# Optimization experiments

Hardware: AMD Instinct MI355X
Metric: run time of the kernel (lower is better)

## Reference

```python
import jax, jax.numpy as jnp
import numpy as np

N_NODES = 50000
N_EDGES = 800000
IN_DIM = 128
HID = 2 * IN_DIM          # GCNConv out channels = input_dims * 2
FC1 = 1024
FC2 = 512
N_ACT = 16
N_AGENTS = 8192
EPS = 1e-5


def setup_inputs() -> dict:
    key = jax.random.key(0)
    ks = jax.random.split(key, 12)
    def gl(k, shape):  # glorot-ish init for weights
        fan = shape[0]
        return jax.random.normal(k, shape, jnp.float32) / jnp.sqrt(jnp.float32(fan))
    return {
        "x": jax.random.normal(ks[0], (N_NODES, IN_DIM), jnp.float32),
        "edge_index": jax.random.randint(ks[1], (2, N_EDGES), 0, N_NODES, jnp.int32),
        "agent_idx": jax.random.randint(ks[2], (N_AGENTS,), 0, N_NODES, jnp.int32),
        "W_gcn": gl(ks[3], (IN_DIM, HID)),
        "b_gcn": jnp.zeros((HID,), jnp.float32),
        "W1": gl(ks[4], (HID, FC1)),
        "b1": jnp.zeros((FC1,), jnp.float32),
        "g1": jnp.ones((FC1,), jnp.float32),
        "be1": jnp.zeros((FC1,), jnp.float32),
        "W2": gl(ks[5], (FC1, FC2)),
        "b2": jnp.zeros((FC2,), jnp.float32),
        "g2": jnp.ones((FC2,), jnp.float32),
        "be2": jnp.zeros((FC2,), jnp.float32),
        "Wmu": gl(ks[6], (FC2, N_ACT)) * 0.003,
        "bmu": jnp.zeros((N_ACT,), jnp.float32),
    }


def _layernorm(h, g, b):
    mu = jnp.mean(h, axis=-1, keepdims=True)
    var = jnp.mean(jnp.square(h - mu), axis=-1, keepdims=True)
    return (h - mu) * jax.lax.rsqrt(var + EPS) * g + b


def _gcn_conv(x, edge_index, W, b):
    # PyG GCNConv: add self-loops, symmetric normalization, linear, scatter-add.
    n = x.shape[0]
    loop = jnp.arange(n, dtype=edge_index.dtype)
    src = jnp.concatenate([edge_index[0], loop])   # [E+N]
    dst = jnp.concatenate([edge_index[1], loop])   # [E+N]
    deg = jax.ops.segment_sum(jnp.ones_like(dst, jnp.float32), dst, num_segments=n)
    dis = jnp.where(deg > 0, jax.lax.rsqrt(jnp.maximum(deg, 1.0)), 0.0)
    norm = dis[src] * dis[dst]                     # [E+N]
    xw = x @ W                                     # [N, HID]
    msg = xw[src] * norm[:, None]                  # gather + scale
    return jax.ops.segment_sum(msg, dst, num_segments=n) + b


def reference(x, edge_index, agent_idx, W_gcn, b_gcn, W1, b1, g1, be1,
              W2, b2, g2, be2, Wmu, bmu):
    h = _gcn_conv(x, edge_index, W_gcn, b_gcn)     # [N, HID]
    h = h[agent_idx]                               # masked selection -> [A, HID]
    h = jax.nn.relu(h)
    h = jax.nn.relu(_layernorm(h @ W1 + b1, g1, be1))
    h = jax.nn.relu(_layernorm(h @ W2 + b2, g2, be2))
    return jax.nn.sigmoid(h @ Wmu + bmu)           # [A, N_ACT]
```

## Files before the change

### kernel.cpp

```cpp
#include <hip/hip_runtime.h>
#include <hip/hip_bf16.h>
#include <math.h>

#define N_NODES  50000
#define N_EDGES  800000
#define IN_DIM   128
#define HID      256
#define FC1      1024
#define FC2      512
#define N_ACT    16
#define N_AGENTS 8192

#define BK       64
#define BM       128
#define BN       128

#define EB_STRIDE    64

#define SCAT_CHUNK   2048
#define SCAT_BLOCKS  ((N_EDGES + SCAT_CHUNK - 1) / SCAT_CHUNK)
#define N_BUCKETS    196
#define BUCKET_CAP   4608
#define WTR_BLOCKS   208
#define CLAIM_BLOCKS (N_AGENTS / 256)

typedef short bf16x8 __attribute__((ext_vector_type(8)));
typedef float floatx4 __attribute__((ext_vector_type(4)));

__device__ __forceinline__ unsigned short f2b(float f) {
    union { float f; unsigned int i; } v;
    v.f = f;
    unsigned int lsb = (v.i >> 16) & 1u;
    v.i += 0x7fffu + lsb;
    return (unsigned short)(v.i >> 16);
}

__device__ __forceinline__ float b2f(unsigned short u) {
    union { unsigned int i; float f; } v;
    v.i = ((unsigned int)u) << 16;
    return v.f;
}

__device__ __forceinline__ void gl_lds(const unsigned short* g, unsigned short* l) {
    __builtin_amdgcn_global_load_lds(
        (const __attribute__((address_space(1))) void*)g,
        (__attribute__((address_space(3))) void*)l, 16, 0, 0);
}

__device__ __forceinline__ void wtr_block(int b, int tid,
    const float* __restrict__ Wgcn, const float* __restrict__ W1,
    const float* __restrict__ W2, const float* __restrict__ Wmu,
    unsigned short* __restrict__ wgcn_t, unsigned short* __restrict__ w1_t,
    unsigned short* __restrict__ w2_t, unsigned short* __restrict__ wmu_t,
    unsigned short (*Ts)[72]) {
    const float* src; unsigned short* dstw; int K, N, tk, tn;
    if (b < 8)        { src = Wgcn; dstw = wgcn_t; K = IN_DIM; N = HID;  tk = b >> 2;        tn = b & 3; }
    else if (b < 72)  { int bb = b - 8;  src = W1; dstw = w1_t; K = HID;  N = FC1;  tk = bb >> 4; tn = bb & 15; }
    else if (b < 200) { int bb = b - 72; src = W2; dstw = w2_t; K = FC1;  N = FC2;  tk = bb >> 3; tn = bb & 7; }
    else              { int bb = b - 200; src = Wmu; dstw = wmu_t; K = FC2; N = N_ACT; tk = bb;   tn = 0; }
    int k0 = tk * 64, n0 = tn * 64;
    int r = tid >> 2;
    int cc = (tid & 3) * 16;
    if (n0 + cc < N) {
        const float* p = src + (size_t)(k0 + r) * N + n0 + cc;
        #pragma unroll
        for (int i = 0; i < 16; i += 4) {
            float4 v = *(const float4*)(p + i);
            Ts[r][cc + i + 0] = f2b(v.x);
            Ts[r][cc + i + 1] = f2b(v.y);
            Ts[r][cc + i + 2] = f2b(v.z);
            Ts[r][cc + i + 3] = f2b(v.w);
        }
    }
    __syncthreads();
    int n = tid >> 2;
    if (n0 + n < N) {
        bf16x8 o0, o1;
        #pragma unroll
        for (int i = 0; i < 8; ++i) o0[i] = (short)Ts[cc + i][n];
        #pragma unroll
        for (int i = 0; i < 8; ++i) o1[i] = (short)Ts[cc + 8 + i][n];
        unsigned short* q = dstw + (size_t)(n0 + n) * K + k0 + cc;
        *(bf16x8*)q = o0;
        *(bf16x8*)(q + 8) = o1;
    }
}

__global__ __launch_bounds__(256) void scat_k(const int* __restrict__ src,
                                              const int* __restrict__ dst,
                                              const int* __restrict__ agent_idx,
                                              int* __restrict__ nid,
                                              int* __restrict__ bcnt,
                                              unsigned long long* __restrict__ pairbuf,
                                              const float* __restrict__ Wgcn,
                                              const float* __restrict__ W1,
                                              const float* __restrict__ W2,
                                              const float* __restrict__ Wmu,
                                              unsigned short* __restrict__ wgcn_t,
                                              unsigned short* __restrict__ w1_t,
                                              unsigned short* __restrict__ w2_t,
                                              unsigned short* __restrict__ wmu_t) {
    __shared__ unsigned short Ts[64][72];
    __shared__ int hist[N_BUCKETS], base_[N_BUCKETS], cur[N_BUCKETS];
    int tid = threadIdx.x;
    int blk = blockIdx.x;
    if (blk >= SCAT_BLOCKS) {
        int bb = blk - SCAT_BLOCKS;
        if (bb < WTR_BLOCKS) {
            wtr_block(bb, tid, Wgcn, W1, W2, Wmu, wgcn_t, w1_t, w2_t, wmu_t, Ts);
        } else {
            int i = (bb - WTR_BLOCKS) * 256 + tid;
            atomicCAS(&nid[agent_idx[i]], 0, i + 1);
        }
        return;
    }
    if (tid < N_BUCKETS) { hist[tid] = 0; cur[tid] = 0; }
    __syncthreads();
    int e0 = blk * SCAT_CHUNK;
    int dv[8];
    #pragma unroll
    for (int i = 0; i < 8; ++i) {
        int e = e0 + i * 256 + tid;
        dv[i] = (e < N_EDGES) ? dst[e] : -1;
        if (dv[i] >= 0) atomicAdd(&hist[dv[i] >> 8], 1);
    }
    __syncthreads();
    if (tid < N_BUCKETS && hist[tid] > 0)
        base_[tid] = atomicAdd(&bcnt[tid], hist[tid]);
    __syncthreads();
    #pragma unroll
    for (int i = 0; i < 8; ++i) {
        int e = e0 + i * 256 + tid;
        if (e < N_EDGES) {
            int d = dv[i];
            int bk = d >> 8;
            int p = base_[bk] + atomicAdd(&cur[bk], 1);
            if (p < BUCKET_CAP)
                pairbuf[(size_t)bk * BUCKET_CAP + p] =
                    ((unsigned long long)(unsigned)src[e] << 32) | (unsigned)d;
        }
    }
}

__global__ __launch_bounds__(256) void bucket_k(const int* __restrict__ bcnt,
                                                const unsigned long long* __restrict__ pairbuf,
                                                const int* __restrict__ nid,
                                                int* __restrict__ deg,
                                                int* __restrict__ ebuf) {
    __shared__ int nidl[256], lhist[256], lfill[256];
    int b = blockIdx.x, tid = threadIdx.x;
    int node = b * 256 + tid;
    nidl[tid] = (node < N_NODES) ? nid[node] : 0;
    lhist[tid] = 0;
    lfill[tid] = 0;
    __syncthreads();
    int n = bcnt[b];
    if (n > BUCKET_CAP) n = BUCKET_CAP;
    const unsigned long long* pb = pairbuf + (size_t)b * BUCKET_CAP;
    for (int i = tid; i < n; i += 256) {
        unsigned long long pr = pb[i];
        int d = (int)(unsigned)pr;
        int s = (int)(pr >> 32);
        int l = d & 255;
        atomicAdd(&lhist[l], 1);
        int cc = nidl[l];
        if (cc != 0) {
            int p = atomicAdd(&lfill[l], 1);
            if (p < EB_STRIDE) ebuf[((cc - 1) << 6) + p] = s;
        }
    }
    __syncthreads();
    if (node < N_NODES) deg[node] = lhist[tid];
}

__global__ __launch_bounds__(256) void accumx_k(const int* __restrict__ agent_idx,
                                                const int* __restrict__ nid,
                                                const int* __restrict__ deg,
                                                const int* __restrict__ ebuf,
                                                const float* __restrict__ x,
                                                unsigned short* __restrict__ agg) {
    int c = blockIdx.x * 4 + (threadIdx.x >> 6);
    int lane = threadIdx.x & 63;
    int n = agent_idx[c];
    float ax = 0.0f, ay = 0.0f;
    if (nid[n] == c + 1) {
        int dn_i = deg[n];
        int cnt = dn_i < EB_STRIDE ? dn_i : EB_STRIDE;
        float dn = rsqrtf((float)(dn_i + 1));
        const int* eb = ebuf + (c << 6);
        int ej = (lane < cnt) ? eb[lane] : n;
        float wl = rsqrtf((float)(deg[ej] + 1)) * dn;
        const float* xl = x + lane * 2;
        int i = 0;
        for (; i + 4 <= cnt; i += 4) {
            int s0 = __shfl(ej, i),     s1 = __shfl(ej, i + 1);
            int s2 = __shfl(ej, i + 2), s3 = __shfl(ej, i + 3);
            float w0 = __shfl(wl, i),     w1 = __shfl(wl, i + 1);
            float w2 = __shfl(wl, i + 2), w3 = __shfl(wl, i + 3);
            float2 u0 = *(const float2*)(xl + (size_t)s0 * IN_DIM);
            float2 u1 = *(const float2*)(xl + (size_t)s1 * IN_DIM);
            float2 u2 = *(const float2*)(xl + (size_t)s2 * IN_DIM);
            float2 u3 = *(const float2*)(xl + (size_t)s3 * IN_DIM);
            ax += w0 * u0.x; ay += w0 * u0.y;
            ax += w1 * u1.x; ay += w1 * u1.y;
            ax += w2 * u2.x; ay += w2 * u2.y;
            ax += w3 * u3.x; ay += w3 * u3.y;
        }
        for (; i < cnt; ++i) {
            int s = __shfl(ej, i);
            float w = __shfl(wl, i);
            float2 u = *(const float2*)(xl + (size_t)s * IN_DIM);
            ax += w * u.x;
            ay += w * u.y;
        }
        float2 u = *(const float2*)(xl + (size_t)n * IN_DIM);
        float w2s = dn * dn;
        ax += w2s * u.x;
        ay += w2s * u.y;
    }
    unsigned int pk = (unsigned int)f2b(ax) | ((unsigned int)f2b(ay) << 16);
    *(unsigned int*)(agg + (size_t)c * IN_DIM + lane * 2) = pk;
}


__global__ __launch_bounds__(256) void gemm_gcn_k(const unsigned short* __restrict__ A,
                                                  const unsigned short* __restrict__ Bt,
                                                  const float* __restrict__ bias,
                                                  unsigned short* __restrict__ outb) {
    __shared__ unsigned short As[64][64];
    __shared__ unsigned short Bs[128][64];
    int bid = blockIdx.x;
    int tn = (bid >> 3) & 1;
    int tm = (bid & 7) + 8 * (bid >> 4);
    int tid = threadIdx.x;
    int lane = tid & 63, wave = tid >> 6;
    int r16 = lane & 15, quad = lane >> 4;
    int lr = (tid >> 3) & 7;
    int swz = ((tid & 7) ^ lr) * 8;
    const int K = IN_DIM, N = HID;

    floatx4 acc[4][2];
    #pragma unroll
    for (int i = 0; i < 4; ++i)
        #pragma unroll
        for (int j = 0; j < 2; ++j)
            acc[i][j] = (floatx4){0.0f, 0.0f, 0.0f, 0.0f};

    for (int k0 = 0; k0 < K; k0 += BK) {
        if (k0) __syncthreads();
        #pragma unroll
        for (int q = 0; q < 2; ++q)
            gl_lds(A + (size_t)(tm * 64 + (wave * 2 + q) * 8 + lr) * K + k0 + swz,
                   &As[(wave * 2 + q) * 8][0]);
        #pragma unroll
        for (int q = 0; q < 4; ++q)
            gl_lds(Bt + (size_t)(tn * 128 + (wave * 4 + q) * 8 + lr) * K + k0 + swz,
                   &Bs[(wave * 4 + q) * 8][0]);
        __syncthreads();
        #pragma unroll
        for (int h = 0; h < 2; ++h) {
            int col = (h * 32 + quad * 8) ^ ((r16 & 7) << 3);
            bf16x8 af[4], bfr[2];
            #pragma unroll
            for (int i = 0; i < 4; ++i)
                af[i] = *(const bf16x8*)&As[i * 16 + r16][col];
            #pragma unroll
            for (int j = 0; j < 2; ++j)
                bfr[j] = *(const bf16x8*)&Bs[wave * 32 + j * 16 + r16][col];
            #pragma unroll
            for (int i = 0; i < 4; ++i)
                #pragma unroll
                for (int j = 0; j < 2; ++j)
                    acc[i][j] = __builtin_amdgcn_mfma_f32_16x16x32_bf16(af[i], bfr[j], acc[i][j], 0, 0, 0);
        }
    }

    #pragma unroll
    for (int j = 0; j < 2; ++j) {
        int ocol = tn * 128 + wave * 32 + j * 16 + r16;
        float bv = bias[ocol];
        #pragma unroll
        for (int i = 0; i < 4; ++i) {
            int orow = tm * 64 + i * 16 + quad * 4;
            #pragma unroll
            for (int r = 0; r < 4; ++r) {
                float v = acc[i][j][r] + bv;
                if (v < 0.0f) v = 0.0f;
                outb[(size_t)(orow + r) * N + ocol] = f2b(v);
            }
        }
    }
}

__global__ __launch_bounds__(256) void gemm_fc1_k(const unsigned short* __restrict__ h_node,
                                                  const int* __restrict__ agent,
                                                  const int* __restrict__ nid,
                                                  const unsigned short* __restrict__ Bt,
                                                  const float* __restrict__ bias,
                                                  unsigned short* __restrict__ outb) {
    __shared__ unsigned short As[BM][64];
    __shared__ unsigned short Bs[BN][64];
    int bid = blockIdx.x;
    int tn = (bid >> 3) & 7;
    int tm = (bid & 7) + 8 * (bid >> 6);
    int tid = threadIdx.x;
    int lane = tid & 63, wave = tid >> 6;
    int wm = wave >> 1, wn = wave & 1;
    int r16 = lane & 15, quad = lane >> 4;
    int lr = (tid >> 3) & 7;
    int swz = ((tid & 7) ^ lr) * 8;
    const int K = HID, N = FC1;

    int cA[4];
    #pragma unroll
    for (int q = 0; q < 4; ++q)
        cA[q] = nid[agent[tm * BM + (wave * 4 + q) * 8 + lr]] - 1;

    floatx4 acc[4][4];
    #pragma unroll
    for (int i = 0; i < 4; ++i)
        #pragma unroll
        for (int j = 0; j < 4; ++j)
            acc[i][j] = (floatx4){0.0f, 0.0f, 0.0f, 0.0f};

    for (int k0 = 0; k0 < K; k0 += BK) {
        if (k0) __syncthreads();
        #pragma unroll
        for (int q = 0; q < 4; ++q) {
            gl_lds(h_node + (size_t)cA[q] * K + k0 + swz,
                   &As[(wave * 4 + q) * 8][0]);
            gl_lds(Bt + (size_t)(tn * BN + (wave * 4 + q) * 8 + lr) * K + k0 + swz,
                   &Bs[(wave * 4 + q) * 8][0]);
        }
        __syncthreads();
        #pragma unroll
        for (int h = 0; h < 2; ++h) {
            int col = (h * 32 + quad * 8) ^ ((r16 & 7) << 3);
            bf16x8 af[4], bfr[4];
            #pragma unroll
            for (int i = 0; i < 4; ++i)
                af[i] = *(const bf16x8*)&As[wm * 64 + i * 16 + r16][col];
            #pragma unroll
            for (int j = 0; j < 4; ++j)
                bfr[j] = *(const bf16x8*)&Bs[wn * 64 + j * 16 + r16][col];
            #pragma unroll
            for (int i = 0; i < 4; ++i)
                #pragma unroll
                for (int j = 0; j < 4; ++j)
                    acc[i][j] = __builtin_amdgcn_mfma_f32_16x16x32_bf16(af[i], bfr[j], acc[i][j], 0, 0, 0);
        }
    }

    float bvj[4];
    #pragma unroll
    for (int j = 0; j < 4; ++j) bvj[j] = bias[tn * BN + wn * 64 + j * 16 + r16];

    #pragma unroll
    for (int i = 0; i < 4; ++i) {
        #pragma unroll
        for (int r = 0; r < 4; ++r) {
            int orow = tm * BM + wm * 64 + i * 16 + quad * 4 + r;
            #pragma unroll
            for (int j = 0; j < 4; ++j) {
                int ocol = tn * BN + wn * 64 + j * 16 + r16;
                outb[(size_t)orow * N + ocol] = f2b(acc[i][j][r] + bvj[j]);
            }
        }
    }
}

__global__ __launch_bounds__(256) void ln1_k(const unsigned short* __restrict__ zb,
                                             const float* __restrict__ g1,
                                             const float* __restrict__ be1,
                                             unsigned short* __restrict__ zbn) {
    int row = blockIdx.x * 4 + (threadIdx.x >> 6);
    int lane = threadIdx.x & 63;
    const unsigned short* p = zb + (size_t)row * FC1 + lane * 16;
    bf16x8 a0 = *(const bf16x8*)p;
    bf16x8 a1 = *(const bf16x8*)(p + 8);
    float v[16];
    #pragma unroll
    for (int i = 0; i < 8; ++i) {
        v[i]     = b2f((unsigned short)a0[i]);
        v[8 + i] = b2f((unsigned short)a1[i]);
    }
    float s = 0.0f, s2 = 0.0f;
    #pragma unroll
    for (int i = 0; i < 16; ++i) { s += v[i]; s2 += v[i] * v[i]; }
    #pragma unroll
    for (int m = 1; m < 64; m <<= 1) {
        s  += __shfl_xor(s, m);
        s2 += __shfl_xor(s2, m);
    }
    float mean = s * (1.0f / FC1);
    float var = s2 * (1.0f / FC1) - mean * mean;
    float inv = rsqrtf(var + 1e-5f);
    const float4* g4 = (const float4*)(g1 + lane * 16);
    const float4* b4 = (const float4*)(be1 + lane * 16);
    float gg[16], bb[16];
    #pragma unroll
    for (int q = 0; q < 4; ++q) {
        float4 gv = g4[q], bv = b4[q];
        gg[q * 4 + 0] = gv.x; gg[q * 4 + 1] = gv.y; gg[q * 4 + 2] = gv.z; gg[q * 4 + 3] = gv.w;
        bb[q * 4 + 0] = bv.x; bb[q * 4 + 1] = bv.y; bb[q * 4 + 2] = bv.z; bb[q * 4 + 3] = bv.w;
    }
    bf16x8 o0, o1;
    #pragma unroll
    for (int i = 0; i < 8; ++i) {
        float w = (v[i] - mean) * inv * gg[i] + bb[i];
        if (w < 0.0f) w = 0.0f;
        o0[i] = (short)f2b(w);
    }
    #pragma unroll
    for (int i = 0; i < 8; ++i) {
        float w = (v[8 + i] - mean) * inv * gg[8 + i] + bb[8 + i];
        if (w < 0.0f) w = 0.0f;
        o1[i] = (short)f2b(w);
    }
    unsigned short* q = zbn + (size_t)row * FC1 + lane * 16;
    *(bf16x8*)q = o0;
    *(bf16x8*)(q + 8) = o1;
}

__global__ __launch_bounds__(256) void gemm_fc2_k(const unsigned short* __restrict__ A,
                                                  const unsigned short* __restrict__ Bt,
                                                  const float* __restrict__ bias,
                                                  unsigned short* __restrict__ outb) {
    __shared__ unsigned short As[BM][64];
    __shared__ unsigned short Bs[BN][64];
    int bid = blockIdx.x;
    int tn = (bid >> 3) & 3;
    int tm = (bid & 7) + 8 * (bid >> 5);
    int tid = threadIdx.x;
    int lane = tid & 63, wave = tid >> 6;
    int wm = wave >> 1, wn = wave & 1;
    int r16 = lane & 15, quad = lane >> 4;
    int lr = (tid >> 3) & 7;
    int swz = ((tid & 7) ^ lr) * 8;
    const int K = FC1, N = FC2;

    floatx4 acc[4][4];
    #pragma unroll
    for (int i = 0; i < 4; ++i)
        #pragma unroll
        for (int j = 0; j < 4; ++j)
            acc[i][j] = (floatx4){0.0f, 0.0f, 0.0f, 0.0f};

    for (int k0 = 0; k0 < K; k0 += BK) {
        if (k0) __syncthreads();
        #pragma unroll
        for (int q = 0; q < 4; ++q) {
            gl_lds(A + (size_t)(tm * BM + (wave * 4 + q) * 8 + lr) * K + k0 + swz,
                   &As[(wave * 4 + q) * 8][0]);
            gl_lds(Bt + (size_t)(tn * BN + (wave * 4 + q) * 8 + lr) * K + k0 + swz,
                   &Bs[(wave * 4 + q) * 8][0]);
        }
        __syncthreads();
        #pragma unroll
        for (int h = 0; h < 2; ++h) {
            int col = (h * 32 + quad * 8) ^ ((r16 & 7) << 3);
            bf16x8 af[4], bfr[4];
            #pragma unroll
            for (int i = 0; i < 4; ++i)
                af[i] = *(const bf16x8*)&As[wm * 64 + i * 16 + r16][col];
            #pragma unroll
            for (int j = 0; j < 4; ++j)
                bfr[j] = *(const bf16x8*)&Bs[wn * 64 + j * 16 + r16][col];
            #pragma unroll
            for (int i = 0; i < 4; ++i)
                #pragma unroll
                for (int j = 0; j < 4; ++j)
                    acc[i][j] = __builtin_amdgcn_mfma_f32_16x16x32_bf16(af[i], bfr[j], acc[i][j], 0, 0, 0);
        }
    }

    float bvj[4];
    #pragma unroll
    for (int j = 0; j < 4; ++j) bvj[j] = bias[tn * BN + wn * 64 + j * 16 + r16];

    #pragma unroll
    for (int i = 0; i < 4; ++i) {
        #pragma unroll
        for (int r = 0; r < 4; ++r) {
            int orow = tm * BM + wm * 64 + i * 16 + quad * 4 + r;
            #pragma unroll
            for (int j = 0; j < 4; ++j) {
                int ocol = tn * BN + wn * 64 + j * 16 + r16;
                outb[(size_t)orow * N + ocol] = f2b(acc[i][j][r] + bvj[j]);
            }
        }
    }
}

__global__ __launch_bounds__(256) void ln2head_k(const unsigned short* __restrict__ z,
                                                 const float* __restrict__ g2,
                                                 const float* __restrict__ be2,
                                                 const unsigned short* __restrict__ wmu_t,
                                                 const float* __restrict__ bmu,
                                                 float* __restrict__ out) {
    __shared__ unsigned short Hs[16][520];
    __shared__ float hred[4][64][4];
    int tid = threadIdx.x;
    int tm = blockIdx.x;
    {
        int row = tid >> 4;
        int sub = tid & 15;
        const unsigned short* src = z + (size_t)(tm * 16 + row) * FC2 + sub * 32;
        bf16x8 a0 = *(const bf16x8*)(src);
        bf16x8 a1 = *(const bf16x8*)(src + 8);
        bf16x8 a2 = *(const bf16x8*)(src + 16);
        bf16x8 a3 = *(const bf16x8*)(src + 24);
        float v[32];
        #pragma unroll
        for (int i = 0; i < 8; ++i) {
            v[i]      = b2f((unsigned short)a0[i]);
            v[8 + i]  = b2f((unsigned short)a1[i]);
            v[16 + i] = b2f((unsigned short)a2[i]);
            v[24 + i] = b2f((unsigned short)a3[i]);
        }
        float s = 0.0f, s2 = 0.0f;
        #pragma unroll
        for (int i = 0; i < 32; ++i) { s += v[i]; s2 += v[i] * v[i]; }
        #pragma unroll
        for (int m = 1; m < 16; m <<= 1) {
            s  += __shfl_xor(s, m);
            s2 += __shfl_xor(s2, m);
        }
        float mean = s * (1.0f / FC2);
        float var = s2 * (1.0f / FC2) - mean * mean;
        float inv = rsqrtf(var + 1e-5f);
        #pragma unroll
        for (int i = 0; i < 32; ++i) {
            int c = sub * 32 + i;
            float w = (v[i] - mean) * inv * g2[c] + be2[c];
            if (w < 0.0f) w = 0.0f;
            Hs[row][c] = f2b(w);
        }
    }
    __syncthreads();
    int lane = tid & 63, wave = tid >> 6;
    int r16 = lane & 15, quad = lane >> 4;
    floatx4 acc = {0.0f, 0.0f, 0.0f, 0.0f};
    #pragma unroll
    for (int st = 0; st < 4; ++st) {
        bf16x8 a = *(const bf16x8*)&Hs[r16][wave * 128 + st * 32 + quad * 8];
        bf16x8 b = *(const bf16x8*)(wmu_t + (size_t)r16 * FC2 + wave * 128 + st * 32 + quad * 8);
        acc = __builtin_amdgcn_mfma_f32_16x16x32_bf16(a, b, acc, 0, 0, 0);
    }
    #pragma unroll
    for (int r = 0; r < 4; ++r) hred[wave][lane][r] = acc[r];
    __syncthreads();
    if (wave == 0) {
        #pragma unroll
        for (int r = 0; r < 4; ++r) {
            float v = hred[0][lane][r] + hred[1][lane][r] + hred[2][lane][r] + hred[3][lane][r];
            v += bmu[r16];
            v = 1.0f / (1.0f + expf(-v));
            out[(size_t)(tm * 16 + quad * 4 + r) * N_ACT + r16] = v;
        }
    }
}

extern "C" void kernel_launch(void* const* d_in, const int* in_sizes, int n_in,
                              void* d_out, int out_size, void* d_ws, size_t ws_size,
                              hipStream_t stream) {
    const float* x    = (const float*)d_in[0];
    const int*   ei   = (const int*)d_in[1];
    const int*   agent= (const int*)d_in[2];
    const float* Wgcn = (const float*)d_in[3];
    const float* bgcn = (const float*)d_in[4];
    const float* W1   = (const float*)d_in[5];
    const float* b1   = (const float*)d_in[6];
    const float* g1   = (const float*)d_in[7];
    const float* be1  = (const float*)d_in[8];
    const float* W2   = (const float*)d_in[9];
    const float* b2   = (const float*)d_in[10];
    const float* g2   = (const float*)d_in[11];
    const float* be2  = (const float*)d_in[12];
    const float* Wmu  = (const float*)d_in[13];
    const float* bmu  = (const float*)d_in[14];
    float* out = (float*)d_out;

    const int* srcp = ei;
    const int* dstp = ei + N_EDGES;

    char* ws = (char*)d_ws;
    size_t off = 0;
    char* zero_base = ws;
    int* nid  = (int*)(ws + off);      off += ((size_t)N_NODES * 4 + 255) & ~(size_t)255;
    int* bcnt = (int*)(ws + off);      off += ((size_t)N_BUCKETS * 4 + 255) & ~(size_t)255;
    size_t zero_bytes = off;
    int* deg  = (int*)(ws + off);      off += ((size_t)N_NODES * 4 + 255) & ~(size_t)255;
    unsigned long long* pairbuf = (unsigned long long*)(ws + off);
    off += ((size_t)N_BUCKETS * BUCKET_CAP * 8 + 255) & ~(size_t)255;
    int* ebuf = (int*)(ws + off);      off += ((size_t)N_AGENTS * EB_STRIDE * 4 + 255) & ~(size_t)255;
    unsigned short* wgcn_t = (unsigned short*)(ws + off); off += ((size_t)IN_DIM * HID * 2 + 255) & ~(size_t)255;
    unsigned short* w1_t   = (unsigned short*)(ws + off); off += ((size_t)HID * FC1 * 2 + 255) & ~(size_t)255;
    unsigned short* w2_t   = (unsigned short*)(ws + off); off += ((size_t)FC1 * FC2 * 2 + 255) & ~(size_t)255;
    unsigned short* wmu_t  = (unsigned short*)(ws + off); off += ((size_t)FC2 * N_ACT * 2 + 255) & ~(size_t)255;
    unsigned short* agg    = (unsigned short*)(ws + off); off += ((size_t)N_AGENTS * IN_DIM * 2 + 255) & ~(size_t)255;
    unsigned short* h_node = (unsigned short*)(ws + off); off += ((size_t)N_AGENTS * HID * 2 + 255) & ~(size_t)255;
    unsigned short* zb  = (unsigned short*)(ws + off);    off += ((size_t)N_AGENTS * FC1 * 2 + 255) & ~(size_t)255;
    unsigned short* zbn = (unsigned short*)(ws + off);    off += ((size_t)N_AGENTS * FC1 * 2 + 255) & ~(size_t)255;
    unsigned short* zb2 = (unsigned short*)(ws + off);    off += ((size_t)N_AGENTS * FC2 * 2 + 255) & ~(size_t)255;

    hipMemsetAsync(zero_base, 0, zero_bytes, stream);

    scat_k<<<SCAT_BLOCKS + WTR_BLOCKS + CLAIM_BLOCKS, 256, 0, stream>>>(
        srcp, dstp, agent, nid, bcnt, pairbuf,
        Wgcn, W1, W2, Wmu, wgcn_t, w1_t, w2_t, wmu_t);

    bucket_k<<<N_BUCKETS, 256, 0, stream>>>(bcnt, pairbuf, nid, deg, ebuf);

    accumx_k<<<N_AGENTS / 4, 256, 0, stream>>>(agent, nid, deg, ebuf, x, agg);

    gemm_gcn_k<<<(HID / 128) * (N_AGENTS / 64), 256, 0, stream>>>(agg, wgcn_t, bgcn, h_node);

    gemm_fc1_k<<<(FC1 / BN) * (N_AGENTS / BM), 256, 0, stream>>>(h_node, agent, nid, w1_t, b1, zb);

    ln1_k<<<N_AGENTS / 4, 256, 0, stream>>>(zb, g1, be1, zbn);

    gemm_fc2_k<<<(FC2 / 128) * (N_AGENTS / 128), 256, 0, stream>>>(zbn, w2_t, b2, zb2);

    ln2head_k<<<N_AGENTS / 16, 256, 0, stream>>>(zb2, g2, be2, wmu_t, bmu, out);
}
```

Before: 180.5 us.

## Fuse LayerNorm1 into FC2 GEMM via FC1 epilogue partial stats; pack edge pairs

The FC1 GEMM epilogue now computes per-row partial sums and sums of squares and writes them to a small stats buffer. The FC2 GEMM reads those stats, applies LayerNorm, affine and ReLU on the fly while staging A into LDS, and prefetches the next A tile in registers. This removes the separate ln1 kernel and the extra write and read of the normalized activation. Separately, the edge bucket buffer now packs source id and local destination into 32 bits instead of 64, halving that traffic. The cost is that the A operand in FC2 no longer uses the direct global-to-LDS path and does per-element normalization math that is repeated for every N tile.

```diff
diff --git a/kernel.cpp b/kernel.cpp
--- a/kernel.cpp
+++ b/kernel.cpp
@@ -91,7 +91,7 @@
                                               const int* __restrict__ agent_idx,
                                               int* __restrict__ nid,
                                               int* __restrict__ bcnt,
-                                              unsigned long long* __restrict__ pairbuf,
+                                              unsigned int* __restrict__ pairbuf,
                                               const float* __restrict__ Wgcn,
                                               const float* __restrict__ W1,
                                               const float* __restrict__ W2,
@@ -137,13 +137,13 @@
             int p = base_[bk] + atomicAdd(&cur[bk], 1);
             if (p < BUCKET_CAP)
                 pairbuf[(size_t)bk * BUCKET_CAP + p] =
-                    ((unsigned long long)(unsigned)src[e] << 32) | (unsigned)d;
+                    ((unsigned int)src[e] << 8) | (unsigned int)(d & 255);
         }
     }
 }
 
 __global__ __launch_bounds__(256) void bucket_k(const int* __restrict__ bcnt,
-                                                const unsigned long long* __restrict__ pairbuf,
+                                                const unsigned int* __restrict__ pairbuf,
                                                 const int* __restrict__ nid,
                                                 int* __restrict__ deg,
                                                 int* __restrict__ ebuf) {
@@ -156,12 +156,11 @@
     __syncthreads();
     int n = bcnt[b];
     if (n > BUCKET_CAP) n = BUCKET_CAP;
-    const unsigned long long* pb = pairbuf + (size_t)b * BUCKET_CAP;
+    const unsigned int* pb = pairbuf + (size_t)b * BUCKET_CAP;
     for (int i = tid; i < n; i += 256) {
-        unsigned long long pr = pb[i];
-        int d = (int)(unsigned)pr;
-        int s = (int)(pr >> 32);
-        int l = d & 255;
+        unsigned int pr = pb[i];
+        int l = (int)(pr & 255u);
+        int s = (int)(pr >> 8);
         atomicAdd(&lhist[l], 1);
         int cc = nidl[l];
         if (cc != 0) {
@@ -297,7 +296,8 @@
                                                   const int* __restrict__ nid,
                                                   const unsigned short* __restrict__ Bt,
                                                   const float* __restrict__ bias,
-                                                  unsigned short* __restrict__ outb) {
+                                                  unsigned short* __restrict__ outb,
+                                                  float2* __restrict__ pstat) {
     __shared__ unsigned short As[BM][64];
     __shared__ unsigned short Bs[BN][64];
     int bid = blockIdx.x;
@@ -360,73 +360,34 @@
         #pragma unroll
         for (int r = 0; r < 4; ++r) {
             int orow = tm * BM + wm * 64 + i * 16 + quad * 4 + r;
+            float vs = 0.0f, vs2 = 0.0f;
             #pragma unroll
             for (int j = 0; j < 4; ++j) {
                 int ocol = tn * BN + wn * 64 + j * 16 + r16;
-                outb[(size_t)orow * N + ocol] = f2b(acc[i][j][r] + bvj[j]);
+                float v = acc[i][j][r] + bvj[j];
+                outb[(size_t)orow * N + ocol] = f2b(v);
+                vs += v;
+                vs2 += v * v;
             }
-        }
-    }
-}
-
-__global__ __launch_bounds__(256) void ln1_k(const unsigned short* __restrict__ zb,
-                                             const float* __restrict__ g1,
-                                             const float* __restrict__ be1,
-                                             unsigned short* __restrict__ zbn) {
-    int row = blockIdx.x * 4 + (threadIdx.x >> 6);
-    int lane = threadIdx.x & 63;
-    const unsigned short* p = zb + (size_t)row * FC1 + lane * 16;
-    bf16x8 a0 = *(const bf16x8*)p;
-    bf16x8 a1 = *(const bf16x8*)(p + 8);
-    float v[16];
-    #pragma unroll
-    for (int i = 0; i < 8; ++i) {
-        v[i]     = b2f((unsigned short)a0[i]);
-        v[8 + i] = b2f((unsigned short)a1[i]);
-    }
-    float s = 0.0f, s2 = 0.0f;
-    #pragma unroll
-    for (int i = 0; i < 16; ++i) { s += v[i]; s2 += v[i] * v[i]; }
-    #pragma unroll
-    for (int m = 1; m < 64; m <<= 1) {
-        s  += __shfl_xor(s, m);
-        s2 += __shfl_xor(s2, m);
-    }
-    float mean = s * (1.0f / FC1);
-    float var = s2 * (1.0f / FC1) - mean * mean;
-    float inv = rsqrtf(var + 1e-5f);
-    const float4* g4 = (const float4*)(g1 + lane * 16);
-    const float4* b4 = (const float4*)(be1 + lane * 16);
-    float gg[16], bb[16];
-    #pragma unroll
-    for (int q = 0; q < 4; ++q) {
-        float4 gv = g4[q], bv = b4[q];
-        gg[q * 4 + 0] = gv.x; gg[q * 4 + 1] = gv.y; gg[q * 4 + 2] = gv.z; gg[q * 4 + 3] = gv.w;
-        bb[q * 4 + 0] = bv.x; bb[q * 4 + 1] = bv.y; bb[q * 4 + 2] = bv.z; bb[q * 4 + 3] = bv.w;
-    }
-    bf16x8 o0, o1;
-    #pragma unroll
-    for (int i = 0; i < 8; ++i) {
-        float w = (v[i] - mean) * inv * gg[i] + bb[i];
-        if (w < 0.0f) w = 0.0f;
-        o0[i] = (short)f2b(w);
-    }
-    #pragma unroll
-    for (int i = 0; i < 8; ++i) {
-        float w = (v[8 + i] - mean) * inv * gg[8 + i] + bb[8 + i];
-        if (w < 0.0f) w = 0.0f;
-        o1[i] = (short)f2b(w);
-    }
-    unsigned short* q = zbn + (size_t)row * FC1 + lane * 16;
-    *(bf16x8*)q = o0;
-    *(bf16x8*)(q + 8) = o1;
-}
-
-__global__ __launch_bounds__(256) void gemm_fc2_k(const unsigned short* __restrict__ A,
-                                                  const unsigned short* __restrict__ Bt,
-                                                  const float* __restrict__ bias,
-                                                  unsigned short* __restrict__ outb) {
-    __shared__ unsigned short As[BM][64];
+            #pragma unroll
+            for (int m = 1; m < 16; m <<= 1) {
+                vs  += __shfl_xor(vs, m);
+                vs2 += __shfl_xor(vs2, m);
+            }
+            if (r16 == 0)
+                pstat[(size_t)orow * 16 + tn * 2 + wn] = make_float2(vs, vs2);
+        }
+    }
+}
+
+__global__ __launch_bounds__(256) void gemm_fc2ln_k(const unsigned short* __restrict__ zb,
+                                                    const float2* __restrict__ pstat,
+                                                    const float* __restrict__ g1,
+                                                    const float* __restrict__ be1,
+                                                    const unsigned short* __restrict__ Bt,
+                                                    const float* __restrict__ bias,
+                                                    unsigned short* __restrict__ outb) {
+    __shared__ unsigned short As[BM][72];
     __shared__ unsigned short Bs[BN][64];
     int bid = blockIdx.x;
     int tn = (bid >> 3) & 3;
@@ -439,6 +400,20 @@
     int swz = ((tid & 7) ^ lr) * 8;
     const int K = FC1, N = FC2;
 
+    int srow2 = tid >> 1;
+    int scol2 = (tid & 1) * 32;
+    int arow = tm * BM + srow2;
+    float s = 0.0f, s2 = 0.0f;
+    {
+        const float2* pp = pstat + (size_t)arow * 16;
+        #pragma unroll
+        for (int t = 0; t < 16; ++t) { float2 p = pp[t]; s += p.x; s2 += p.y; }
+    }
+    float mean = s * (1.0f / FC1);
+    float var = s2 * (1.0f / FC1) - mean * mean;
+    float inv = rsqrtf(var + 1e-5f);
+    const unsigned short* pa = zb + (size_t)arow * K + scol2;
+
     floatx4 acc[4][4];
     #pragma unroll
     for (int i = 0; i < 4; ++i)
@@ -446,26 +421,45 @@
         for (int j = 0; j < 4; ++j)
             acc[i][j] = (floatx4){0.0f, 0.0f, 0.0f, 0.0f};
 
+    bf16x8 ra[4];
+    #pragma unroll
+    for (int cc = 0; cc < 4; ++cc) ra[cc] = *(const bf16x8*)(pa + cc * 8);
+
     for (int k0 = 0; k0 < K; k0 += BK) {
         if (k0) __syncthreads();
         #pragma unroll
-        for (int q = 0; q < 4; ++q) {
-            gl_lds(A + (size_t)(tm * BM + (wave * 4 + q) * 8 + lr) * K + k0 + swz,
-                   &As[(wave * 4 + q) * 8][0]);
+        for (int cc = 0; cc < 4; ++cc) {
+            bf16x8 o;
+            #pragma unroll
+            for (int kx = 0; kx < 8; ++kx) {
+                int gk = k0 + scol2 + cc * 8 + kx;
+                float v = (b2f((unsigned short)ra[cc][kx]) - mean) * inv * g1[gk] + be1[gk];
+                if (v < 0.0f) v = 0.0f;
+                o[kx] = (short)f2b(v);
+            }
+            *(bf16x8*)&As[srow2][scol2 + cc * 8] = o;
+        }
+        #pragma unroll
+        for (int q = 0; q < 4; ++q)
             gl_lds(Bt + (size_t)(tn * BN + (wave * 4 + q) * 8 + lr) * K + k0 + swz,
                    &Bs[(wave * 4 + q) * 8][0]);
+        if (k0 + BK < K) {
+            #pragma unroll
+            for (int cc = 0; cc < 4; ++cc)
+                ra[cc] = *(const bf16x8*)(pa + k0 + BK + cc * 8);
         }
         __syncthreads();
         #pragma unroll
         for (int h = 0; h < 2; ++h) {
-            int col = (h * 32 + quad * 8) ^ ((r16 & 7) << 3);
+            int colA = h * 32 + quad * 8;
+            int colB = colA ^ ((r16 & 7) << 3);
             bf16x8 af[4], bfr[4];
             #pragma unroll
             for (int i = 0; i < 4; ++i)
-                af[i] = *(const bf16x8*)&As[wm * 64 + i * 16 + r16][col];
+                af[i] = *(const bf16x8*)&As[wm * 64 + i * 16 + r16][colA];
             #pragma unroll
             for (int j = 0; j < 4; ++j)
-                bfr[j] = *(const bf16x8*)&Bs[wn * 64 + j * 16 + r16][col];
+                bfr[j] = *(const bf16x8*)&Bs[wn * 64 + j * 16 + r16][colB];
             #pragma unroll
             for (int i = 0; i < 4; ++i)
                 #pragma unroll
@@ -591,9 +585,10 @@
     int* bcnt = (int*)(ws + off);      off += ((size_t)N_BUCKETS * 4 + 255) & ~(size_t)255;
     size_t zero_bytes = off;
     int* deg  = (int*)(ws + off);      off += ((size_t)N_NODES * 4 + 255) & ~(size_t)255;
-    unsigned long long* pairbuf = (unsigned long long*)(ws + off);
-    off += ((size_t)N_BUCKETS * BUCKET_CAP * 8 + 255) & ~(size_t)255;
+    unsigned int* pairbuf = (unsigned int*)(ws + off);
+    off += ((size_t)N_BUCKETS * BUCKET_CAP * 4 + 255) & ~(size_t)255;
     int* ebuf = (int*)(ws + off);      off += ((size_t)N_AGENTS * EB_STRIDE * 4 + 255) & ~(size_t)255;
+    float2* pstat = (float2*)(ws + off); off += ((size_t)N_AGENTS * 16 * 8 + 255) & ~(size_t)255;
     unsigned short* wgcn_t = (unsigned short*)(ws + off); off += ((size_t)IN_DIM * HID * 2 + 255) & ~(size_t)255;
     unsigned short* w1_t   = (unsigned short*)(ws + off); off += ((size_t)HID * FC1 * 2 + 255) & ~(size_t)255;
     unsigned short* w2_t   = (unsigned short*)(ws + off); off += ((size_t)FC1 * FC2 * 2 + 255) & ~(size_t)255;
@@ -601,7 +596,6 @@
     unsigned short* agg    = (unsigned short*)(ws + off); off += ((size_t)N_AGENTS * IN_DIM * 2 + 255) & ~(size_t)255;
     unsigned short* h_node = (unsigned short*)(ws + off); off += ((size_t)N_AGENTS * HID * 2 + 255) & ~(size_t)255;
     unsigned short* zb  = (unsigned short*)(ws + off);    off += ((size_t)N_AGENTS * FC1 * 2 + 255) & ~(size_t)255;
-    unsigned short* zbn = (unsigned short*)(ws + off);    off += ((size_t)N_AGENTS * FC1 * 2 + 255) & ~(size_t)255;
     unsigned short* zb2 = (unsigned short*)(ws + off);    off += ((size_t)N_AGENTS * FC2 * 2 + 255) & ~(size_t)255;
 
     hipMemsetAsync(zero_base, 0, zero_bytes, stream);
@@ -616,11 +610,11 @@
 
     gemm_gcn_k<<<(HID / 128) * (N_AGENTS / 64), 256, 0, stream>>>(agg, wgcn_t, bgcn, h_node);
 
-    gemm_fc1_k<<<(FC1 / BN) * (N_AGENTS / BM), 256, 0, stream>>>(h_node, agent, nid, w1_t, b1, zb);
-
-    ln1_k<<<N_AGENTS / 4, 256, 0, stream>>>(zb, g1, be1, zbn);
-
-    gemm_fc2_k<<<(FC2 / 128) * (N_AGENTS / 128), 256, 0, stream>>>(zbn, w2_t, b2, zb2);
+    gemm_fc1_k<<<(FC1 / BN) * (N_AGENTS / BM), 256, 0, stream>>>(h_node, agent, nid, w1_t, b1,
+                                                                 zb, pstat);
+
+    gemm_fc2ln_k<<<(FC2 / 128) * (N_AGENTS / 128), 256, 0, stream>>>(zb, pstat, g1, be1,
+                                                                     w2_t, b2, zb2);
 
     ln2head_k<<<N_AGENTS / 16, 256, 0, stream>>>(zb2, g2, be2, wmu_t, bmu, out);
 }
```

After: 198.2 us. 9.8% more time.
